# Performance work log

Hardware: AMD Instinct MI355X
Metric: run time of the kernel (lower is better)

Reference implementation:

```python
import jax, jax.numpy as jnp
import numpy as np

NUM_NODES = 10000
NUM_EDGES = 640000
IN_CH = 128
HID = 128
OUT_CH = 1


def setup_inputs() -> dict:
    key = jax.random.key(0)
    ks = jax.random.split(key, 12)
    x = jax.random.normal(ks[0], (NUM_NODES, IN_CH), dtype=jnp.float32)
    edge_index = jax.random.randint(ks[1], (2, NUM_EDGES), 0, NUM_NODES, dtype=jnp.int64)
    edge_weight = jax.random.uniform(ks[2], (NUM_EDGES,), dtype=jnp.float32)
    s1 = 1.0 / np.sqrt(IN_CH)
    s2 = 1.0 / np.sqrt(HID)
    W1 = jax.random.uniform(ks[3], (HID, IN_CH), minval=-s1, maxval=s1, dtype=jnp.float32)
    b1 = jnp.zeros((HID,), dtype=jnp.float32)
    W2 = jax.random.uniform(ks[4], (HID, HID), minval=-s2, maxval=s2, dtype=jnp.float32)
    b2 = jnp.zeros((HID,), dtype=jnp.float32)
    sc = 1.0 / np.sqrt(HID * 3)
    conv_w = jax.random.uniform(ks[5], (HID, HID, 3), minval=-sc, maxval=sc, dtype=jnp.float32)
    conv_b = jax.random.uniform(ks[6], (HID,), minval=-sc, maxval=sc, dtype=jnp.float32)
    fc_w = jax.random.uniform(ks[7], (OUT_CH, HID), minval=-s2, maxval=s2, dtype=jnp.float32)
    fc_b = jax.random.uniform(ks[8], (OUT_CH,), minval=-s2, maxval=s2, dtype=jnp.float32)
    return {"x": x, "edge_index": edge_index, "edge_weight": edge_weight,
            "W1": W1, "b1": b1, "W2": W2, "b2": b2,
            "conv_w": conv_w, "conv_b": conv_b, "fc_w": fc_w, "fc_b": fc_b}


def _gcn_conv(x, row, col, norm, W, b):
    # PyG GCNConv: linear (no bias in lin), normalized scatter-add, then bias
    xw = x @ W.T                                   # [N, out]
    msg = xw[row] * norm[:, None]                  # gather + edge scale [E, out]
    out = jax.ops.segment_sum(msg, col, num_segments=NUM_NODES)
    return out + b


def reference(x, edge_index, edge_weight, W1, b1, W2, b2, conv_w, conv_b, fc_w, fc_b):
    # gcn_norm with self-loops (fill_value=1.0)
    loop = jnp.arange(NUM_NODES, dtype=edge_index.dtype)
    row = jnp.concatenate([edge_index[0], loop])
    col = jnp.concatenate([edge_index[1], loop])
    w = jnp.concatenate([edge_weight, jnp.ones((NUM_NODES,), dtype=edge_weight.dtype)])
    deg = jax.ops.segment_sum(w, col, num_segments=NUM_NODES)
    dinv = jnp.where(deg > 0, jax.lax.rsqrt(deg), 0.0)
    norm = dinv[row] * w * dinv[col]

    h = jax.nn.relu(_gcn_conv(x, row, col, norm, W1, b1))
    # dropout is identity in eval mode
    h = jax.nn.relu(_gcn_conv(h, row, col, norm, W2, b2))

    # temporal conv1d over node axis: [N,H] -> [1,H,N]
    hc = h.T[None, :, :]
    hc = jax.lax.conv_general_dilated(hc, conv_w, window_strides=(1,),
                                      padding='SAME',
                                      dimension_numbers=('NCH', 'OIH', 'NCH'))
    hc = hc + conv_b[None, :, None]
    h = hc[0].T                                    # [N, H]

    return (h @ fc_w.T + fc_b).squeeze()           # [N]
```

## Files before the change

### kernel.cpp

```cpp
#include <hip/hip_runtime.h>
#include <hip/hip_bf16.h>

#define N_NODES 10000
#define N_EDGES 640000
#define CH 128
#define NB 256
#define EPB (N_EDGES / NB)
#define NCHUNK 40

__global__ __launch_bounds__(256) void fused_hist_gemm(const int* __restrict__ ei,
        const float* __restrict__ x, const float* __restrict__ W1,
        int* __restrict__ hist, float* __restrict__ out) {
    __shared__ __align__(16) char smem[40000];
    int t = threadIdx.x;
    if (blockIdx.x < NB) {
        int* h = (int*)smem;
        int b = blockIdx.x;
        for (int i = t; i < N_NODES; i += 256) h[i] = 0;
        __syncthreads();
        int e0 = b * EPB;
        for (int i = t; i < EPB; i += 256)
            atomicAdd(&h[ei[N_EDGES + e0 + i]], 1);
        __syncthreads();
        for (int i = t; i < N_NODES; i += 256)
            hist[b * N_NODES + i] = h[i];
        return;
    }
    float (*As)[68]  = (float(*)[68])smem;
    float (*Ws)[132] = (float(*)[132])(smem + 32 * 68 * sizeof(float));
    int tx = t & 31;
    int ty = t >> 5;
    int row0 = (blockIdx.x - NB) * 64;
    float acc[8][4] = {};
    for (int k0 = 0; k0 < 128; k0 += 32) {
        #pragma unroll
        for (int i = 0; i < 8; ++i) {
            int idx = t + i * 256;
            int r = idx >> 5, k = idx & 31;
            int gr = row0 + r;
            As[k][r] = (gr < N_NODES) ? x[gr * CH + k0 + k] : 0.0f;
        }
        #pragma unroll
        for (int i = 0; i < 16; ++i) {
            int idx = t + i * 256;
            int o = idx >> 5, k = idx & 31;
            Ws[k][o] = W1[o * CH + k0 + k];
        }
        __syncthreads();
        #pragma unroll
        for (int kk = 0; kk < 32; ++kk) {
            float a[8], w[4];
            #pragma unroll
            for (int j = 0; j < 8; ++j) a[j] = As[kk][ty * 8 + j];
            #pragma unroll
            for (int c = 0; c < 4; ++c) w[c] = Ws[kk][tx * 4 + c];
            #pragma unroll
            for (int j = 0; j < 8; ++j)
                #pragma unroll
                for (int c = 0; c < 4; ++c)
                    acc[j][c] += a[j] * w[c];
        }
        __syncthreads();
    }
    #pragma unroll
    for (int j = 0; j < 8; ++j) {
        int gr = row0 + ty * 8 + j;
        if (gr < N_NODES) {
            float4 v = make_float4(acc[j][0], acc[j][1], acc[j][2], acc[j][3]);
            *reinterpret_cast<float4*>(&out[gr * CH + tx * 4]) = v;
        }
    }
}

__global__ __launch_bounds__(256) void reduce_kernel(const int* __restrict__ hist,
        int* __restrict__ tot, int* __restrict__ csum,
        const float* __restrict__ conv_w, const float* __restrict__ conv_b,
        const float* __restrict__ fc_w, const float* __restrict__ fc_b,
        float* __restrict__ vbuf, float* __restrict__ c0) {
    int blk = blockIdx.x, t = threadIdx.x;
    if (blk == NCHUNK) {
        for (int i = t; i <= 384; i += 256) {
            if (i < 384) {
                float s = 0.0f;
                for (int o = 0; o < CH; ++o) s += fc_w[o] * conv_w[o * 384 + i];
                vbuf[i] = s;
            } else {
                float s = fc_b[0];
                for (int o = 0; o < CH; ++o) s += fc_w[o] * conv_b[o];
                *c0 = s;
            }
        }
        return;
    }
    int n = blk * 256 + t;
    int c = 0;
    if (n < N_NODES) {
        #pragma unroll 8
        for (int b = 0; b < NB; ++b) c += hist[b * N_NODES + n];
        tot[n] = c;
    }
    __shared__ int wred[4];
    int lane = t & 63, wave = t >> 6;
    int s = c;
    #pragma unroll
    for (int off = 32; off > 0; off >>= 1) s += __shfl_down(s, off, 64);
    if (lane == 0) wred[wave] = s;
    __syncthreads();
    if (t == 0) csum[blk] = wred[0] + wred[1] + wred[2] + wred[3];
}

__global__ __launch_bounds__(256) void bofs_kernel(int* __restrict__ hist,
        const int* __restrict__ tot, const int* __restrict__ csum,
        int* __restrict__ offs) {
    __shared__ int lds_csum[NCHUNK];
    __shared__ int wsum[4];
    int blk = blockIdx.x, t = threadIdx.x;
    if (t < NCHUNK) lds_csum[t] = csum[t];
    __syncthreads();
    int base = 0;
    for (int i = 0; i < blk; ++i) base += lds_csum[i];
    int n = blk * 256 + t;
    int v = (n < N_NODES) ? tot[n] : 0;
    int lane = t & 63, wave = t >> 6;
    int s = v;
    #pragma unroll
    for (int off = 1; off < 64; off <<= 1) {
        int u = __shfl_up(s, off, 64);
        if (lane >= off) s += u;
    }
    if (lane == 63) wsum[wave] = s;
    __syncthreads();
    int wbase = 0;
    for (int i = 0; i < wave; ++i) wbase += wsum[i];
    if (n < N_NODES) {
        int run = base + wbase + s - v;
        offs[n] = run;
        for (int b = 0; b < NB; ++b) {
            int h = hist[b * N_NODES + n];
            hist[b * N_NODES + n] = run;
            run += h;
        }
    }
}

__global__ __launch_bounds__(256) void scatter_kernel(const int* __restrict__ ei,
        const float* __restrict__ ew, const int* __restrict__ bofs,
        int2* __restrict__ erec) {
    __shared__ int cur[N_NODES];
    int b = blockIdx.x, t = threadIdx.x;
    for (int i = t; i < N_NODES; i += 256) cur[i] = bofs[b * N_NODES + i];
    __syncthreads();
    int e0 = b * EPB;
    for (int i = t; i < EPB; i += 256) {
        int e = e0 + i;
        int r = ei[e];
        int c = ei[N_EDGES + e];
        int p = atomicAdd(&cur[c], 1);
        erec[p] = make_int2(r, __float_as_int(ew[e]));
    }
}

__global__ __launch_bounds__(256) void deg_kernel(const int2* __restrict__ erec,
        const int* __restrict__ offs, const int* __restrict__ cnt,
        float* __restrict__ dinv) {
    int n = blockIdx.x * 8 + (threadIdx.x >> 5);
    int l = threadIdx.x & 31;
    int start = offs[n];
    int num = cnt[n];
    float s = 0.0f;
    for (int i = l; i < num; i += 32) s += __int_as_float(erec[start + i].y);
    #pragma unroll
    for (int off = 16; off > 0; off >>= 1) s += __shfl_down(s, off, 32);
    if (l == 0) dinv[n] = rsqrtf(s + 1.0f);
}

__global__ __launch_bounds__(256) void gemm128_kernel(const float* __restrict__ A,
                                                      const float* __restrict__ W,
                                                      float* __restrict__ out, int M) {
    __shared__ float As[32][68];
    __shared__ float Ws[32][132];
    int tid = threadIdx.x;
    int tx = tid & 31;
    int ty = tid >> 5;
    int row0 = blockIdx.x * 64;
    float acc[8][4] = {};
    for (int k0 = 0; k0 < 128; k0 += 32) {
        #pragma unroll
        for (int i = 0; i < 8; ++i) {
            int idx = tid + i * 256;
            int r = idx >> 5, k = idx & 31;
            int gr = row0 + r;
            As[k][r] = (gr < M) ? A[gr * CH + k0 + k] : 0.0f;
        }
        #pragma unroll
        for (int i = 0; i < 16; ++i) {
            int idx = tid + i * 256;
            int o = idx >> 5, k = idx & 31;
            Ws[k][o] = W[o * CH + k0 + k];
        }
        __syncthreads();
        #pragma unroll
        for (int kk = 0; kk < 32; ++kk) {
            float a[8], w[4];
            #pragma unroll
            for (int j = 0; j < 8; ++j) a[j] = As[kk][ty * 8 + j];
            #pragma unroll
            for (int c = 0; c < 4; ++c) w[c] = Ws[kk][tx * 4 + c];
            #pragma unroll
            for (int j = 0; j < 8; ++j)
                #pragma unroll
                for (int c = 0; c < 4; ++c)
                    acc[j][c] += a[j] * w[c];
        }
        __syncthreads();
    }
    #pragma unroll
    for (int j = 0; j < 8; ++j) {
        int gr = row0 + ty * 8 + j;
        if (gr < M) {
            float4 v = make_float4(acc[j][0], acc[j][1], acc[j][2], acc[j][3]);
            *reinterpret_cast<float4*>(&out[gr * CH + tx * 4]) = v;
        }
    }
}

__global__ __launch_bounds__(256) void agg_kernel(const float4* __restrict__ xw4,
        const int2* __restrict__ erec, const int* __restrict__ offs,
        const int* __restrict__ cnt, const float* __restrict__ dinv,
        const float4* __restrict__ bias4, float4* __restrict__ out4) {
    int l = threadIdx.x & 31;
    int g = threadIdx.x >> 5;
    int n = blockIdx.x * 8 + g;
    float d = dinv[n];
    float4 self = xw4[n * 32 + l];
    float4 acc = make_float4(d * self.x, d * self.y, d * self.z, d * self.w);
    int start = offs[n];
    int num = cnt[n];
    int i = 0;
    for (; i + 8 <= num; i += 8) {
        int2 r[8];
        #pragma unroll
        for (int j = 0; j < 8; ++j) r[j] = erec[start + i + j];
        float4 f[8];
        float dr[8];
        #pragma unroll
        for (int j = 0; j < 8; ++j) f[j] = xw4[r[j].x * 32 + l];
        #pragma unroll
        for (int j = 0; j < 8; ++j) dr[j] = dinv[r[j].x];
        #pragma unroll
        for (int j = 0; j < 8; ++j) {
            float v = __int_as_float(r[j].y) * dr[j];
            acc.x += v * f[j].x; acc.y += v * f[j].y;
            acc.z += v * f[j].z; acc.w += v * f[j].w;
        }
    }
    for (; i < num; ++i) {
        int2 r = erec[start + i];
        float4 f = xw4[r.x * 32 + l];
        float v = __int_as_float(r.y) * dinv[r.x];
        acc.x += v * f.x; acc.y += v * f.y; acc.z += v * f.z; acc.w += v * f.w;
    }
    float4 bb = bias4[l];
    acc.x = fmaxf(d * acc.x + bb.x, 0.0f);
    acc.y = fmaxf(d * acc.y + bb.y, 0.0f);
    acc.z = fmaxf(d * acc.z + bb.z, 0.0f);
    acc.w = fmaxf(d * acc.w + bb.w, 0.0f);
    out4[n * 32 + l] = acc;
}

__global__ __launch_bounds__(256) void convfc_kernel(const float* __restrict__ h,
        const float* __restrict__ v, const float* __restrict__ c0,
        float* __restrict__ out, int N) {
    int n = blockIdx.x * 4 + (threadIdx.x >> 6);
    int l = threadIdx.x & 63;
    if (n >= N) return;
    const float* hn = h + n * CH;
    float v0a = v[l * 3 + 0],        v1a = v[l * 3 + 1],        v2a = v[l * 3 + 2];
    float v0b = v[(l + 64) * 3 + 0], v1b = v[(l + 64) * 3 + 1], v2b = v[(l + 64) * 3 + 2];
    float p = hn[l] * v1a + hn[l + 64] * v1b;
    if (n > 0)     p += hn[l - CH] * v0a + hn[l + 64 - CH] * v0b;
    if (n < N - 1) p += hn[l + CH] * v2a + hn[l + 64 + CH] * v2b;
    #pragma unroll
    for (int off = 32; off > 0; off >>= 1) p += __shfl_down(p, off, 64);
    if (l == 0) out[n] = p + *c0;
}

extern "C" void kernel_launch(void* const* d_in, const int* in_sizes, int n_in,
                              void* d_out, int out_size, void* d_ws, size_t ws_size,
                              hipStream_t stream) {
    const float* x       = (const float*)d_in[0];
    const int*   ei      = (const int*)d_in[1];
    const float* ew      = (const float*)d_in[2];
    const float* W1      = (const float*)d_in[3];
    const float* b1      = (const float*)d_in[4];
    const float* W2      = (const float*)d_in[5];
    const float* b2      = (const float*)d_in[6];
    const float* conv_w  = (const float*)d_in[7];
    const float* conv_b  = (const float*)d_in[8];
    const float* fc_w    = (const float*)d_in[9];
    const float* fc_b    = (const float*)d_in[10];
    float* out = (float*)d_out;

    float* bufA   = (float*)d_ws;
    float* bufB   = bufA + N_NODES * CH;
    int2*  erec   = (int2*)(bufB + N_NODES * CH);
    int*   hist   = (int*)(erec + N_EDGES);
    int*   tot    = hist + NB * N_NODES;
    int*   offs   = tot + N_NODES;
    float* dinv   = (float*)(offs + N_NODES);
    float* vbuf   = dinv + N_NODES;
    float* c0     = vbuf + 384;
    int*   csum   = (int*)(c0 + 1);

    const int gemm_grid = (N_NODES + 63) / 64;

    fused_hist_gemm<<<NB + gemm_grid, 256, 0, stream>>>(ei, x, W1, hist, bufA);
    reduce_kernel<<<NCHUNK + 1, 256, 0, stream>>>(hist, tot, csum,
                                                  conv_w, conv_b, fc_w, fc_b, vbuf, c0);
    bofs_kernel<<<NCHUNK, 256, 0, stream>>>(hist, tot, csum, offs);
    scatter_kernel<<<NB, 256, 0, stream>>>(ei, ew, hist, erec);
    deg_kernel<<<N_NODES / 8, 256, 0, stream>>>(erec, offs, tot, dinv);

    agg_kernel<<<N_NODES / 8, 256, 0, stream>>>((const float4*)bufA, erec, offs, tot,
                                                dinv, (const float4*)b1, (float4*)bufB);
    gemm128_kernel<<<gemm_grid, 256, 0, stream>>>(bufB, W2, bufA, N_NODES);
    agg_kernel<<<N_NODES / 8, 256, 0, stream>>>((const float4*)bufA, erec, offs, tot,
                                                dinv, (const float4*)b2, (float4*)bufB);
    convfc_kernel<<<(N_NODES + 3) / 4, 256, 0, stream>>>(bufB, vbuf, c0, out, N_NODES);
}
```

Baseline: 225.5 us.

## Fold reduce kernel into hist/GEMM launch and cut histogram blocks to 64

Reduces the number of per-block histograms from 256 to 64, shrinking the histogram buffer and the per-node column sums in the offset pass. Each histogram block also emits per-chunk partial sums, which lets the separate reduce kernel be removed: the conv/fc weight folding moves into an extra block of the fused launch, and the chunk base is computed inside the offset kernel. This saves one launch and a large read of the histogram buffer. In exchange, each histogram and scatter block now handles four times as many edges, which means more LDS atomic contention per block and less parallelism in those stages.

```diff
diff --git a/kernel.cpp b/kernel.cpp
--- a/kernel.cpp
+++ b/kernel.cpp
@@ -4,81 +4,41 @@
 #define N_NODES 10000
 #define N_EDGES 640000
 #define CH 128
-#define NB 256
+#define NB 64
 #define EPB (N_EDGES / NB)
 #define NCHUNK 40
+#define NPAD 10240
 
 __global__ __launch_bounds__(256) void fused_hist_gemm(const int* __restrict__ ei,
         const float* __restrict__ x, const float* __restrict__ W1,
-        int* __restrict__ hist, float* __restrict__ out) {
-    __shared__ __align__(16) char smem[40000];
-    int t = threadIdx.x;
-    if (blockIdx.x < NB) {
-        int* h = (int*)smem;
-        int b = blockIdx.x;
-        for (int i = t; i < N_NODES; i += 256) h[i] = 0;
-        __syncthreads();
-        int e0 = b * EPB;
-        for (int i = t; i < EPB; i += 256)
-            atomicAdd(&h[ei[N_EDGES + e0 + i]], 1);
-        __syncthreads();
-        for (int i = t; i < N_NODES; i += 256)
-            hist[b * N_NODES + i] = h[i];
-        return;
-    }
-    float (*As)[68]  = (float(*)[68])smem;
-    float (*Ws)[132] = (float(*)[132])(smem + 32 * 68 * sizeof(float));
-    int tx = t & 31;
-    int ty = t >> 5;
-    int row0 = (blockIdx.x - NB) * 64;
-    float acc[8][4] = {};
-    for (int k0 = 0; k0 < 128; k0 += 32) {
-        #pragma unroll
-        for (int i = 0; i < 8; ++i) {
-            int idx = t + i * 256;
-            int r = idx >> 5, k = idx & 31;
-            int gr = row0 + r;
-            As[k][r] = (gr < N_NODES) ? x[gr * CH + k0 + k] : 0.0f;
-        }
-        #pragma unroll
-        for (int i = 0; i < 16; ++i) {
-            int idx = t + i * 256;
-            int o = idx >> 5, k = idx & 31;
-            Ws[k][o] = W1[o * CH + k0 + k];
-        }
-        __syncthreads();
-        #pragma unroll
-        for (int kk = 0; kk < 32; ++kk) {
-            float a[8], w[4];
-            #pragma unroll
-            for (int j = 0; j < 8; ++j) a[j] = As[kk][ty * 8 + j];
-            #pragma unroll
-            for (int c = 0; c < 4; ++c) w[c] = Ws[kk][tx * 4 + c];
-            #pragma unroll
-            for (int j = 0; j < 8; ++j)
-                #pragma unroll
-                for (int c = 0; c < 4; ++c)
-                    acc[j][c] += a[j] * w[c];
-        }
-        __syncthreads();
-    }
-    #pragma unroll
-    for (int j = 0; j < 8; ++j) {
-        int gr = row0 + ty * 8 + j;
-        if (gr < N_NODES) {
-            float4 v = make_float4(acc[j][0], acc[j][1], acc[j][2], acc[j][3]);
-            *reinterpret_cast<float4*>(&out[gr * CH + tx * 4]) = v;
-        }
-    }
-}
-
-__global__ __launch_bounds__(256) void reduce_kernel(const int* __restrict__ hist,
-        int* __restrict__ tot, int* __restrict__ csum,
+        int* __restrict__ hist, int* __restrict__ pcs, float* __restrict__ out,
         const float* __restrict__ conv_w, const float* __restrict__ conv_b,
         const float* __restrict__ fc_w, const float* __restrict__ fc_b,
         float* __restrict__ vbuf, float* __restrict__ c0) {
-    int blk = blockIdx.x, t = threadIdx.x;
-    if (blk == NCHUNK) {
+    __shared__ __align__(16) char smem[NPAD * 4];
+    int t = threadIdx.x;
+    int bid = blockIdx.x;
+    if (bid < NB) {
+        int* h = (int*)smem;
+        for (int i = t; i < NPAD; i += 256) h[i] = 0;
+        __syncthreads();
+        int e0 = bid * EPB;
+        for (int i = t; i < EPB; i += 256)
+            atomicAdd(&h[ei[N_EDGES + e0 + i]], 1);
+        __syncthreads();
+        for (int i = t; i < N_NODES; i += 256)
+            hist[bid * N_NODES + i] = h[i];
+        int lane = t & 63, wave = t >> 6;
+        for (int cch = wave; cch < NCHUNK; cch += 4) {
+            int s = h[cch * 256 + lane] + h[cch * 256 + lane + 64]
+                  + h[cch * 256 + lane + 128] + h[cch * 256 + lane + 192];
+            #pragma unroll
+            for (int off = 32; off > 0; off >>= 1) s += __shfl_down(s, off, 64);
+            if (lane == 0) pcs[cch * NB + bid] = s;
+        }
+        return;
+    }
+    if (bid == NB + (N_NODES + 63) / 64) {
         for (int i = t; i <= 384; i += 256) {
             if (i < 384) {
                 float s = 0.0f;
@@ -92,36 +52,74 @@
         }
         return;
     }
+    float (*As)[68]  = (float(*)[68])smem;
+    float (*Ws)[132] = (float(*)[132])(smem + 32 * 68 * sizeof(float));
+    int tx = t & 31;
+    int ty = t >> 5;
+    int row0 = (bid - NB) * 64;
+    float acc[8][4] = {};
+    for (int k0 = 0; k0 < 128; k0 += 32) {
+        #pragma unroll
+        for (int i = 0; i < 8; ++i) {
+            int idx = t + i * 256;
+            int r = idx >> 5, k = idx & 31;
+            int gr = row0 + r;
+            As[k][r] = (gr < N_NODES) ? x[gr * CH + k0 + k] : 0.0f;
+        }
+        #pragma unroll
+        for (int i = 0; i < 16; ++i) {
+            int idx = t + i * 256;
+            int o = idx >> 5, k = idx & 31;
+            Ws[k][o] = W1[o * CH + k0 + k];
+        }
+        __syncthreads();
+        #pragma unroll
+        for (int kk = 0; kk < 32; ++kk) {
+            float a[8], w[4];
+            #pragma unroll
+            for (int j = 0; j < 8; ++j) a[j] = As[kk][ty * 8 + j];
+            #pragma unroll
+            for (int c = 0; c < 4; ++c) w[c] = Ws[kk][tx * 4 + c];
+            #pragma unroll
+            for (int j = 0; j < 8; ++j)
+                #pragma unroll
+                for (int c = 0; c < 4; ++c)
+                    acc[j][c] += a[j] * w[c];
+        }
+        __syncthreads();
+    }
+    #pragma unroll
+    for (int j = 0; j < 8; ++j) {
+        int gr = row0 + ty * 8 + j;
+        if (gr < N_NODES) {
+            float4 v = make_float4(acc[j][0], acc[j][1], acc[j][2], acc[j][3]);
+            *reinterpret_cast<float4*>(&out[gr * CH + tx * 4]) = v;
+        }
+    }
+}
+
+__global__ __launch_bounds__(256) void bofs_kernel(int* __restrict__ hist,
+        const int* __restrict__ pcs, int* __restrict__ tot,
+        int* __restrict__ offs) {
+    __shared__ int wred[4];
+    __shared__ int wsum[4];
+    __shared__ int base_sh;
+    int blk = blockIdx.x, t = threadIdx.x;
+    int lane = t & 63, wave = t >> 6;
+    int bsum = 0;
+    for (int i = t; i < blk * NB; i += 256) bsum += pcs[i];
+    #pragma unroll
+    for (int off = 32; off > 0; off >>= 1) bsum += __shfl_down(bsum, off, 64);
+    if (lane == 0) wred[wave] = bsum;
+    __syncthreads();
+    if (t == 0) base_sh = wred[0] + wred[1] + wred[2] + wred[3];
     int n = blk * 256 + t;
-    int c = 0;
+    int v = 0;
     if (n < N_NODES) {
         #pragma unroll 8
-        for (int b = 0; b < NB; ++b) c += hist[b * N_NODES + n];
-        tot[n] = c;
-    }
-    __shared__ int wred[4];
-    int lane = t & 63, wave = t >> 6;
-    int s = c;
-    #pragma unroll
-    for (int off = 32; off > 0; off >>= 1) s += __shfl_down(s, off, 64);
-    if (lane == 0) wred[wave] = s;
-    __syncthreads();
-    if (t == 0) csum[blk] = wred[0] + wred[1] + wred[2] + wred[3];
-}
-
-__global__ __launch_bounds__(256) void bofs_kernel(int* __restrict__ hist,
-        const int* __restrict__ tot, const int* __restrict__ csum,
-        int* __restrict__ offs) {
-    __shared__ int lds_csum[NCHUNK];
-    __shared__ int wsum[4];
-    int blk = blockIdx.x, t = threadIdx.x;
-    if (t < NCHUNK) lds_csum[t] = csum[t];
-    __syncthreads();
-    int base = 0;
-    for (int i = 0; i < blk; ++i) base += lds_csum[i];
-    int n = blk * 256 + t;
-    int v = (n < N_NODES) ? tot[n] : 0;
-    int lane = t & 63, wave = t >> 6;
+        for (int b = 0; b < NB; ++b) v += hist[b * N_NODES + n];
+        tot[n] = v;
+    }
     int s = v;
     #pragma unroll
     for (int off = 1; off < 64; off <<= 1) {
@@ -133,7 +131,7 @@
     int wbase = 0;
     for (int i = 0; i < wave; ++i) wbase += wsum[i];
     if (n < N_NODES) {
-        int run = base + wbase + s - v;
+        int run = base_sh + wbase + s - v;
         offs[n] = run;
         for (int b = 0; b < NB; ++b) {
             int h = hist[b * N_NODES + n];
@@ -305,19 +303,18 @@
     float* bufB   = bufA + N_NODES * CH;
     int2*  erec   = (int2*)(bufB + N_NODES * CH);
     int*   hist   = (int*)(erec + N_EDGES);
-    int*   tot    = hist + NB * N_NODES;
+    int*   pcs    = hist + NB * N_NODES;
+    int*   tot    = pcs + NCHUNK * NB;
     int*   offs   = tot + N_NODES;
     float* dinv   = (float*)(offs + N_NODES);
     float* vbuf   = dinv + N_NODES;
     float* c0     = vbuf + 384;
-    int*   csum   = (int*)(c0 + 1);
 
     const int gemm_grid = (N_NODES + 63) / 64;
 
-    fused_hist_gemm<<<NB + gemm_grid, 256, 0, stream>>>(ei, x, W1, hist, bufA);
-    reduce_kernel<<<NCHUNK + 1, 256, 0, stream>>>(hist, tot, csum,
-                                                  conv_w, conv_b, fc_w, fc_b, vbuf, c0);
-    bofs_kernel<<<NCHUNK, 256, 0, stream>>>(hist, tot, csum, offs);
+    fused_hist_gemm<<<NB + gemm_grid + 1, 256, 0, stream>>>(ei, x, W1, hist, pcs,
+            bufA, conv_w, conv_b, fc_w, fc_b, vbuf, c0);
+    bofs_kernel<<<NCHUNK, 256, 0, stream>>>(hist, pcs, tot, offs);
     scatter_kernel<<<NB, 256, 0, stream>>>(ei, ew, hist, erec);
     deg_kernel<<<N_NODES / 8, 256, 0, stream>>>(erec, offs, tot, dinv);
 
```

Result: faster. 219.5 us (-2.7%).
